# Performance work log

Hardware: AMD Instinct MI355X
Metric: run time of the kernel (lower is better)

Reference implementation:

```python
import jax, jax.numpy as jnp
import numpy as np

D_MODEL = 1024
NHEAD = 16
HEAD_DIM = D_MODEL // NHEAD
B, T = 2, 2048


def setup_inputs() -> dict:
    key = jax.random.key(0)
    ks = jax.random.split(key, 11)
    s = 1.0 / np.sqrt(D_MODEL)
    inp = {
        'q': jax.random.normal(ks[0], (B, T, D_MODEL), jnp.float32),
        'k': jax.random.normal(ks[1], (B, T, D_MODEL), jnp.float32),
        'v': jax.random.normal(ks[2], (B, T, D_MODEL), jnp.float32),
        'Wq': jax.random.normal(ks[3], (D_MODEL, D_MODEL), jnp.float32) * s,
        'bq': jnp.zeros((D_MODEL,), jnp.float32),
        'Wk': jax.random.normal(ks[4], (D_MODEL, D_MODEL), jnp.float32) * s,
        'bk': jnp.zeros((D_MODEL,), jnp.float32),
        'Wv': jax.random.normal(ks[5], (D_MODEL, D_MODEL), jnp.float32) * s,
        'bv': jnp.zeros((D_MODEL,), jnp.float32),
        'Wo': jax.random.normal(ks[6], (D_MODEL, D_MODEL), jnp.float32) * s,
        'bo': jnp.zeros((D_MODEL,), jnp.float32),
    }
    return inp


def reference(q, k, v, Wq, bq, Wk, bk, Wv, bv, Wo, bo):
    scale = np.sqrt(HEAD_DIM).astype(np.float32)
    # projections (torch Linear: x @ W.T + b), split heads -> [B, H, T, Dh]
    def proj(x, W, b):
        y = jnp.einsum('btd,ed->bte', x, W) + b
        return y.reshape(B, T, NHEAD, HEAD_DIM).transpose(0, 2, 1, 3)
    qh = proj(q, Wq, bq)
    kh = proj(k, Wk, bk)
    vh = proj(v, Wv, bv)
    scores = jnp.einsum('bhqd,bhkd->bhqk', qh, kh) / scale  # [B,H,T,T]
    weights = jax.nn.softmax(scores, axis=-1)
    out = jnp.einsum('bhqk,bhkd->bhqd', weights, vh)        # [B,H,T,Dh]
    out = out.transpose(0, 2, 1, 3).reshape(B, T, D_MODEL)
    return jnp.einsum('btd,ed->bte', out, Wo) + bo
```

## Files before the change

### kernel.cpp

```cpp
#include <hip/hip_runtime.h>
#include <cstdint>
#include <cstddef>


#define D_MODEL 1024
#define NHEAD   16
#define HDIM    64
#define BATCH   2
#define SEQ     2048
#define BT      (BATCH * SEQ)

#define QSCALE 0.18033688011112043f

typedef __bf16 bf16;
typedef __bf16 bf16x8 __attribute__((ext_vector_type(8)));
typedef __bf16 bf16x4 __attribute__((ext_vector_type(4)));
typedef float  floatx4 __attribute__((ext_vector_type(4)));
typedef short  short4v __attribute__((ext_vector_type(4)));

#define MFMA16(a, b, c) __builtin_amdgcn_mfma_f32_16x16x32_bf16((a), (b), (c), 0, 0, 0)

__device__ __forceinline__ floatx4 MFMA16B(bf16x4 a, bf16x4 b, floatx4 c) {
  return __builtin_amdgcn_mfma_f32_16x16x16bf16_1k(
      __builtin_bit_cast(short4v, a), __builtin_bit_cast(short4v, b), c, 0, 0, 0);
}

__device__ __forceinline__ float fexp2(float x) {
  return __builtin_amdgcn_exp2f(x);
}

__device__ __forceinline__ void async_cp16(const bf16* g, bf16* l) {
  __builtin_amdgcn_global_load_lds(
      (__attribute__((address_space(1))) void*)(g),
      (__attribute__((address_space(3))) void*)(l), 16, 0, 0);
}

__global__ __launch_bounds__(256) void cvt7(
    const float* __restrict__ s0, const float* __restrict__ s1,
    const float* __restrict__ s2, const float* __restrict__ s3,
    const float* __restrict__ s4, const float* __restrict__ s5,
    const float* __restrict__ s6,
    bf16* __restrict__ d0, bf16* __restrict__ d1, bf16* __restrict__ d2,
    bf16* __restrict__ d3, bf16* __restrict__ d4, bf16* __restrict__ d5,
    bf16* __restrict__ d6)
{
  const float* src; bf16* dst; int n4;
  switch (blockIdx.y) {
    case 0:  src = s0; dst = d0; n4 = (BT * D_MODEL) / 4; break;
    case 1:  src = s1; dst = d1; n4 = (BT * D_MODEL) / 4; break;
    case 2:  src = s2; dst = d2; n4 = (BT * D_MODEL) / 4; break;
    case 3:  src = s3; dst = d3; n4 = (D_MODEL * D_MODEL) / 4; break;
    case 4:  src = s4; dst = d4; n4 = (D_MODEL * D_MODEL) / 4; break;
    case 5:  src = s5; dst = d5; n4 = (D_MODEL * D_MODEL) / 4; break;
    default: src = s6; dst = d6; n4 = (D_MODEL * D_MODEL) / 4; break;
  }
  int stride = gridDim.x * blockDim.x;
  for (int i = blockIdx.x * blockDim.x + threadIdx.x; i < n4; i += stride) {
    float4 f = ((const float4*)src)[i];
    bf16x4 h;
    h[0] = (bf16)f.x; h[1] = (bf16)f.y; h[2] = (bf16)f.z; h[3] = (bf16)f.w;
    ((bf16x4*)dst)[i] = h;
  }
}

__device__ __forceinline__ void gemm128_core(
    const bf16* __restrict__ A, const bf16* __restrict__ W,
    int m0, int n0, bf16* As, bf16* Bs, floatx4 acc[4][4])
{
  const int t = threadIdx.x;
  const int l = t & 63, w = t >> 6;
  const int quad = l >> 4, lr = l & 15;
  const int wm = (w >> 1) * 64, wn = (w & 1) * 64;

  floatx4 z = {0.f, 0.f, 0.f, 0.f};
#pragma unroll
  for (int i = 0; i < 4; i++)
#pragma unroll
    for (int j = 0; j < 4; j++) acc[i][j] = z;

  for (int kt = 0; kt < 1024; kt += 32) {
    __syncthreads();
#pragma unroll
    for (int i = 0; i < 2; i++) {
      int c = i * 256 + t;
      int row = c >> 2, ci = c & 3;
      async_cp16(A + (size_t)(m0 + row) * 1024 + kt + ci * 8,
                 As + (i * 256 + w * 64) * 8);
      async_cp16(W + (size_t)(n0 + row) * 1024 + kt + ci * 8,
                 Bs + (i * 256 + w * 64) * 8);
    }
    __syncthreads();

    bf16x8 af[4], bfr[4];
#pragma unroll
    for (int i = 0; i < 4; i++) {
      af[i]  = *(const bf16x8*)(As + (wm + i * 16 + lr) * 32 + quad * 8);
      bfr[i] = *(const bf16x8*)(Bs + (wn + i * 16 + lr) * 32 + quad * 8);
    }
#pragma unroll
    for (int i = 0; i < 4; i++)
#pragma unroll
      for (int j = 0; j < 4; j++)
        acc[i][j] = MFMA16(af[i], bfr[j], acc[i][j]);
  }
}

__global__ __launch_bounds__(256) void qkv_gemm(
    const bf16* __restrict__ qb, const bf16* __restrict__ kb, const bf16* __restrict__ vb,
    const bf16* __restrict__ wq, const bf16* __restrict__ wk, const bf16* __restrict__ wv,
    const float* __restrict__ biasq, const float* __restrict__ biask, const float* __restrict__ biasv,
    bf16* __restrict__ qh, bf16* __restrict__ kh, bf16* __restrict__ vt)
{
  __shared__ bf16 As[128 * 32];
  __shared__ bf16 Bs[128 * 32];
  const int zid = blockIdx.z;
  const bf16* A = (zid == 0) ? qb : ((zid == 1) ? kb : vb);
  const bf16* W = (zid == 0) ? wq : ((zid == 1) ? wk : wv);
  const float* bias = (zid == 0) ? biasq : ((zid == 1) ? biask : biasv);
  const int m0 = blockIdx.x * 128, n0 = blockIdx.y * 128;

  floatx4 acc[4][4];
  gemm128_core(A, W, m0, n0, As, Bs, acc);

  const int t = threadIdx.x, l = t & 63, w = t >> 6;
  const int quad = l >> 4, lr = l & 15;
  const int wm = (w >> 1) * 64, wn = (w & 1) * 64;
  const float sc = (zid == 0) ? QSCALE : 1.0f;

  if (zid < 2) {
    bf16* out = (zid == 0) ? qh : kh;
#pragma unroll
    for (int i = 0; i < 4; i++) {
      int mbase = m0 + wm + i * 16 + quad * 4;
      int b  = mbase >> 11;
      int tq = mbase & 2047;
#pragma unroll
      for (int j = 0; j < 4; j++) {
        int n = n0 + wn + j * 16 + lr;
        float bv = bias[n];
        int h = n >> 6, dh = n & 63;
        bf16* p = out + ((size_t)((b * NHEAD + h) * SEQ + tq)) * HDIM + dh;
#pragma unroll
        for (int r = 0; r < 4; r++)
          p[(size_t)r * HDIM] = (bf16)((acc[i][j][r] + bv) * sc);
      }
    }
  } else {
#pragma unroll
    for (int i = 0; i < 4; i++) {
      int mbase = m0 + wm + i * 16 + quad * 4;
      int b  = mbase >> 11;
      int tq = mbase & 2047;
#pragma unroll
      for (int j = 0; j < 4; j++) {
        int n = n0 + wn + j * 16 + lr;
        float bv = bias[n];
        int h = n >> 6, dh = n & 63;
        bf16x4 pk;
#pragma unroll
        for (int r = 0; r < 4; r++) pk[r] = (bf16)(acc[i][j][r] + bv);
        *(bf16x4*)(vt + ((size_t)((b * NHEAD + h) * HDIM + dh)) * SEQ + tq) = pk;
      }
    }
  }
}

__global__ __launch_bounds__(256, 2) void attn_fused(
    const bf16* __restrict__ qh, const bf16* __restrict__ kh,
    const bf16* __restrict__ vt, bf16* __restrict__ attn)
{
  __shared__ __align__(16) char smem[65536];

  const int t = threadIdx.x, l = t & 63, w = t >> 6;
  const int quad = l >> 4, lr = l & 15;
  const int bh = blockIdx.y;
  const int qt0 = blockIdx.x * 128;
  const bf16* qg = qh + (size_t)bh * SEQ * HDIM;
  const bf16* kg = kh + (size_t)bh * SEQ * HDIM;
  const bf16* vg = vt + (size_t)bh * HDIM * SEQ;

  const bf16* kseg[4];
  const bf16* vseg[4];
#pragma unroll
  for (int i = 0; i < 4; i++) {
    int s = w * 4 + i;
    int krow = s * 8 + (l >> 3);
    kseg[i] = kg + (size_t)krow * HDIM + (((l & 7) ^ (l >> 3)) * 8);
    int vrow = s * 4 + (l >> 4);
    vseg[i] = vg + (size_t)vrow * SEQ + (((l & 15) ^ (vrow & 15)) * 8);
  }

  bf16x8 qf[2][2];
#pragma unroll
  for (int g = 0; g < 2; g++)
#pragma unroll
    for (int ko = 0; ko < 2; ko++)
      qf[g][ko] = *(const bf16x8*)(qg + (size_t)(qt0 + w * 32 + g * 16 + lr) * HDIM
                                   + ko * 32 + quad * 8);

  const floatx4 zz = {0.f, 0.f, 0.f, 0.f};
  floatx4 Oacc[2][4];
#pragma unroll
  for (int g = 0; g < 2; g++)
#pragma unroll
    for (int dt = 0; dt < 4; dt++) Oacc[g][dt] = zz;
  float mrow[2] = {-3.0e38f, -3.0e38f};
  float lrow[2] = {0.f, 0.f};

  auto stage = [&](int buf, int kt) {
    bf16* Kb = (bf16*)(smem + buf * 32768);
    bf16* Vb = (bf16*)(smem + buf * 32768 + 16384);
    int off = kt * 128;
#pragma unroll
    for (int i = 0; i < 4; i++) {
      async_cp16(kseg[i] + (size_t)off * HDIM, Kb + (w * 4 + i) * 512);
      async_cp16(vseg[i] + off,                Vb + (w * 4 + i) * 512);
    }
  };

  stage(0, 0);

  for (int kt = 0; kt < 16; kt++) {
    const int p = kt & 1;
    __syncthreads();
    if (kt + 1 < 16) stage(1 - p, kt + 1);
    const bf16* Ks  = (const bf16*)(smem + p * 32768);
    const bf16* Vts = (const bf16*)(smem + p * 32768 + 16384);

    const bf16* krow0 = Ks + lr * 64 + ((quad ^ (lr & 7)) * 8);
    const bf16* krow1 = Ks + lr * 64 + (((quad + 4) ^ (lr & 7)) * 8);

    floatx4 s0[8], s1[8];
#pragma unroll
    for (int ni = 0; ni < 8; ni++) {
      bf16x8 k0 = *(const bf16x8*)(krow0 + ni * 1024);
      bf16x8 k1 = *(const bf16x8*)(krow1 + ni * 1024);
      floatx4 a0 = MFMA16(k0, qf[0][0], zz);
      a0 = MFMA16(k1, qf[0][1], a0);
      floatx4 a1 = MFMA16(k0, qf[1][0], zz);
      a1 = MFMA16(k1, qf[1][1], a1);
      s0[ni] = a0;
      s1[ni] = a1;
    }

    bf16x4 pk0[8], pk1[8];
#pragma unroll
    for (int g = 0; g < 2; g++) {
      floatx4* sg = g ? s1 : s0;
      bf16x4* pkg = g ? pk1 : pk0;
      float rmax = sg[0][0];
#pragma unroll
      for (int ni = 0; ni < 8; ni++)
#pragma unroll
        for (int r = 0; r < 4; r++) rmax = fmaxf(rmax, sg[ni][r]);
      rmax = fmaxf(rmax, __shfl_xor(rmax, 16, 64));
      rmax = fmaxf(rmax, __shfl_xor(rmax, 32, 64));
      if (!__all(rmax - mrow[g] <= 8.0f)) {
        float mnew = fmaxf(mrow[g], rmax);
        float al = fexp2(mrow[g] - mnew);
        mrow[g] = mnew;
        lrow[g] *= al;
#pragma unroll
        for (int dt = 0; dt < 4; dt++)
#pragma unroll
          for (int r = 0; r < 4; r++) Oacc[g][dt][r] *= al;
      }
      float m = mrow[g];
      float rsum = 0.f;
#pragma unroll
      for (int ni = 0; ni < 8; ni++)
#pragma unroll
        for (int r = 0; r < 4; r++) {
          float pv = fexp2(sg[ni][r] - m);
          rsum += pv;
          pkg[ni][r] = (bf16)pv;
        }
      rsum += __shfl_xor(rsum, 16, 64);
      rsum += __shfl_xor(rsum, 32, 64);
      lrow[g] += rsum;
    }

    const bf16* vbase = Vts + lr * 128 + (quad & 1) * 4;
#pragma unroll
    for (int ni = 0; ni < 8; ni++) {
      const bf16* vp = vbase + (((ni * 2 + (quad >> 1)) ^ lr) * 8);
#pragma unroll
      for (int dt = 0; dt < 4; dt++) {
        bf16x4 vf = *(const bf16x4*)(vp + dt * 2048);
        Oacc[0][dt] = MFMA16B(vf, pk0[ni], Oacc[0][dt]);
        Oacc[1][dt] = MFMA16B(vf, pk1[ni], Oacc[1][dt]);
      }
    }
  }

  bf16* Ost = (bf16*)smem;
#pragma unroll
  for (int g = 0; g < 2; g++) {
    float inv = 1.0f / lrow[g];
#pragma unroll
    for (int dt = 0; dt < 4; dt++) {
      bf16x4 ov;
#pragma unroll
      for (int r = 0; r < 4; r++) ov[r] = (bf16)(Oacc[g][dt][r] * inv);
      *(bf16x4*)(Ost + (size_t)(w * 32 + g * 16 + lr) * 72 + dt * 16 + quad * 4) = ov;
    }
  }
  __syncthreads();

  const int b = bh >> 4, h = bh & 15;
#pragma unroll
  for (int i = 0; i < 4; i++) {
    int c = t + 256 * i;
    int row = c >> 3, ci = c & 7;
    *(int4*)(attn + ((size_t)b * SEQ + qt0 + row) * D_MODEL + h * HDIM + ci * 8) =
        *(const int4*)(Ost + row * 72 + ci * 8);
  }
}

__global__ __launch_bounds__(256) void oproj_gemm(
    const bf16* __restrict__ attn, const bf16* __restrict__ wo,
    const float* __restrict__ bo, float* __restrict__ out)
{
  __shared__ bf16 As[64 * 32];
  __shared__ bf16 Bs[64 * 32];
  const int m0 = blockIdx.x * 64, n0 = blockIdx.y * 64;
  const int t = threadIdx.x, l = t & 63, w = t >> 6;
  const int quad = l >> 4, lr = l & 15;
  const int wm = (w >> 1) * 32, wn = (w & 1) * 32;

  floatx4 z = {0.f, 0.f, 0.f, 0.f};
  floatx4 acc[2][2];
#pragma unroll
  for (int i = 0; i < 2; i++)
#pragma unroll
    for (int j = 0; j < 2; j++) acc[i][j] = z;

  for (int kt = 0; kt < 1024; kt += 32) {
    __syncthreads();
    {
      int row = t >> 2, ci = t & 3;
      async_cp16(attn + (size_t)(m0 + row) * 1024 + kt + ci * 8,
                 As + (w * 64) * 8);
      async_cp16(wo + (size_t)(n0 + row) * 1024 + kt + ci * 8,
                 Bs + (w * 64) * 8);
    }
    __syncthreads();

    bf16x8 af[2], bfr[2];
#pragma unroll
    for (int i = 0; i < 2; i++) {
      af[i]  = *(const bf16x8*)(As + (wm + i * 16 + lr) * 32 + quad * 8);
      bfr[i] = *(const bf16x8*)(Bs + (wn + i * 16 + lr) * 32 + quad * 8);
    }
#pragma unroll
    for (int i = 0; i < 2; i++)
#pragma unroll
      for (int j = 0; j < 2; j++)
        acc[i][j] = MFMA16(af[i], bfr[j], acc[i][j]);
  }

#pragma unroll
  for (int i = 0; i < 2; i++) {
    int m = m0 + wm + i * 16 + quad * 4;
#pragma unroll
    for (int j = 0; j < 2; j++) {
      int n = n0 + wn + j * 16 + lr;
      float bv = bo[n];
      float* p = out + (size_t)m * D_MODEL + n;
#pragma unroll
      for (int r = 0; r < 4; r++)
        p[(size_t)r * D_MODEL] = acc[i][j][r] + bv;
    }
  }
}

extern "C" void kernel_launch(void* const* d_in, const int* in_sizes, int n_in,
                              void* d_out, int out_size, void* d_ws, size_t ws_size,
                              hipStream_t stream)
{
  const float* q  = (const float*)d_in[0];
  const float* k  = (const float*)d_in[1];
  const float* v  = (const float*)d_in[2];
  const float* Wq = (const float*)d_in[3];
  const float* bq = (const float*)d_in[4];
  const float* Wk = (const float*)d_in[5];
  const float* bk = (const float*)d_in[6];
  const float* Wv = (const float*)d_in[7];
  const float* bv = (const float*)d_in[8];
  const float* Wo = (const float*)d_in[9];
  const float* bo = (const float*)d_in[10];

  const size_t NQ = (size_t)BT * D_MODEL;
  const size_t NW = (size_t)D_MODEL * D_MODEL;

  bf16* p = (bf16*)d_ws;
  bf16* qb   = p; p += NQ;
  bf16* kb   = p; p += NQ;
  bf16* vb   = p; p += NQ;
  bf16* wqb  = p; p += NW;
  bf16* wkb  = p; p += NW;
  bf16* wvb  = p; p += NW;
  bf16* wob  = p; p += NW;
  bf16* qhp  = p; p += NQ;
  bf16* khp  = p; p += NQ;
  bf16* vtp  = p; p += NQ;
  bf16* attn = p; p += NQ;

  cvt7<<<dim3(1024, 7, 1), 256, 0, stream>>>(q, k, v, Wq, Wk, Wv, Wo,
                                             qb, kb, vb, wqb, wkb, wvb, wob);
  qkv_gemm<<<dim3(32, 8, 3), 256, 0, stream>>>(qb, kb, vb, wqb, wkb, wvb,
                                               bq, bk, bv, qhp, khp, vtp);
  attn_fused<<<dim3(16, 32, 1), 256, 0, stream>>>(qhp, khp, vtp, attn);
  oproj_gemm<<<dim3(64, 16, 1), 256, 0, stream>>>(attn, wob, bo, (float*)d_out);
}
```

Measured before the change: 223.6 us.

## Remap attention blocks, interleave softmax reductions, and raise MFMA wave priority

Remaps the linear block index so that consecutive blocks cover different heads and batches at the same query tile. This is meant to change how K/V tiles are shared in L2 across concurrently running blocks. The softmax max and sum reductions are rewritten as tree reductions that handle both row groups together, giving the scheduler more independent work. MFMA sequences are wrapped in s_setprio and V fragment loads are hoisted so matrix ops issue back-to-back, while the reordered dependent MFMAs give more latency hiding. The risks are that the remapping assumes the grid is exactly 16 by 32 blocks, and that the priority hints may have little effect.

```diff
diff --git a/kernel.cpp b/kernel.cpp
--- a/kernel.cpp
+++ b/kernel.cpp
@@ -173,8 +173,12 @@
 
   const int t = threadIdx.x, l = t & 63, w = t >> 6;
   const int quad = l >> 4, lr = l & 15;
-  const int bh = blockIdx.y;
-  const int qt0 = blockIdx.x * 128;
+
+  const int hb  = blockIdx.y * 16 + blockIdx.x;
+  const int j   = hb >> 3;
+  const int bh  = (hb & 7) + ((j & 3) << 3);
+  const int qt0 = (j >> 2) * 128;
+
   const bf16* qg = qh + (size_t)bh * SEQ * HDIM;
   const bf16* kg = kh + (size_t)bh * SEQ * HDIM;
   const bf16* vg = vt + (size_t)bh * HDIM * SEQ;
@@ -235,61 +239,97 @@
     for (int ni = 0; ni < 8; ni++) {
       bf16x8 k0 = *(const bf16x8*)(krow0 + ni * 1024);
       bf16x8 k1 = *(const bf16x8*)(krow1 + ni * 1024);
+      __builtin_amdgcn_s_setprio(1);
       floatx4 a0 = MFMA16(k0, qf[0][0], zz);
+      floatx4 a1 = MFMA16(k0, qf[1][0], zz);
       a0 = MFMA16(k1, qf[0][1], a0);
-      floatx4 a1 = MFMA16(k0, qf[1][0], zz);
       a1 = MFMA16(k1, qf[1][1], a1);
+      __builtin_amdgcn_s_setprio(0);
       s0[ni] = a0;
       s1[ni] = a1;
     }
 
+    float xm0[8], xm1[8];
+#pragma unroll
+    for (int ni = 0; ni < 8; ni++) {
+      xm0[ni] = fmaxf(fmaxf(s0[ni][0], s0[ni][1]), fmaxf(s0[ni][2], s0[ni][3]));
+      xm1[ni] = fmaxf(fmaxf(s1[ni][0], s1[ni][1]), fmaxf(s1[ni][2], s1[ni][3]));
+    }
+    float r0 = fmaxf(fmaxf(fmaxf(xm0[0], xm0[1]), fmaxf(xm0[2], xm0[3])),
+                     fmaxf(fmaxf(xm0[4], xm0[5]), fmaxf(xm0[6], xm0[7])));
+    float r1 = fmaxf(fmaxf(fmaxf(xm1[0], xm1[1]), fmaxf(xm1[2], xm1[3])),
+                     fmaxf(fmaxf(xm1[4], xm1[5]), fmaxf(xm1[6], xm1[7])));
+    r0 = fmaxf(r0, __shfl_xor(r0, 16, 64));
+    r1 = fmaxf(r1, __shfl_xor(r1, 16, 64));
+    r0 = fmaxf(r0, __shfl_xor(r0, 32, 64));
+    r1 = fmaxf(r1, __shfl_xor(r1, 32, 64));
+
+    if (!__all(r0 - mrow[0] <= 8.0f)) {
+      float mnew = fmaxf(mrow[0], r0);
+      float al = fexp2(mrow[0] - mnew);
+      mrow[0] = mnew;
+      lrow[0] *= al;
+#pragma unroll
+      for (int dt = 0; dt < 4; dt++)
+#pragma unroll
+        for (int r = 0; r < 4; r++) Oacc[0][dt][r] *= al;
+    }
+    if (!__all(r1 - mrow[1] <= 8.0f)) {
+      float mnew = fmaxf(mrow[1], r1);
+      float al = fexp2(mrow[1] - mnew);
+      mrow[1] = mnew;
+      lrow[1] *= al;
+#pragma unroll
+      for (int dt = 0; dt < 4; dt++)
+#pragma unroll
+        for (int r = 0; r < 4; r++) Oacc[1][dt][r] *= al;
+    }
+
+    const float m0v = mrow[0], m1v = mrow[1];
     bf16x4 pk0[8], pk1[8];
-#pragma unroll
-    for (int g = 0; g < 2; g++) {
-      floatx4* sg = g ? s1 : s0;
-      bf16x4* pkg = g ? pk1 : pk0;
-      float rmax = sg[0][0];
-#pragma unroll
-      for (int ni = 0; ni < 8; ni++)
-#pragma unroll
-        for (int r = 0; r < 4; r++) rmax = fmaxf(rmax, sg[ni][r]);
-      rmax = fmaxf(rmax, __shfl_xor(rmax, 16, 64));
-      rmax = fmaxf(rmax, __shfl_xor(rmax, 32, 64));
-      if (!__all(rmax - mrow[g] <= 8.0f)) {
-        float mnew = fmaxf(mrow[g], rmax);
-        float al = fexp2(mrow[g] - mnew);
-        mrow[g] = mnew;
-        lrow[g] *= al;
-#pragma unroll
-        for (int dt = 0; dt < 4; dt++)
-#pragma unroll
-          for (int r = 0; r < 4; r++) Oacc[g][dt][r] *= al;
-      }
-      float m = mrow[g];
-      float rsum = 0.f;
-#pragma unroll
-      for (int ni = 0; ni < 8; ni++)
-#pragma unroll
-        for (int r = 0; r < 4; r++) {
-          float pv = fexp2(sg[ni][r] - m);
-          rsum += pv;
-          pkg[ni][r] = (bf16)pv;
-        }
-      rsum += __shfl_xor(rsum, 16, 64);
-      rsum += __shfl_xor(rsum, 32, 64);
-      lrow[g] += rsum;
-    }
+    float t0[8], t1[8];
+#pragma unroll
+    for (int ni = 0; ni < 8; ni++) {
+      float p00 = fexp2(s0[ni][0] - m0v), p01 = fexp2(s0[ni][1] - m0v);
+      float p02 = fexp2(s0[ni][2] - m0v), p03 = fexp2(s0[ni][3] - m0v);
+      float p10 = fexp2(s1[ni][0] - m1v), p11 = fexp2(s1[ni][1] - m1v);
+      float p12 = fexp2(s1[ni][2] - m1v), p13 = fexp2(s1[ni][3] - m1v);
+      pk0[ni][0] = (bf16)p00; pk0[ni][1] = (bf16)p01;
+      pk0[ni][2] = (bf16)p02; pk0[ni][3] = (bf16)p03;
+      pk1[ni][0] = (bf16)p10; pk1[ni][1] = (bf16)p11;
+      pk1[ni][2] = (bf16)p12; pk1[ni][3] = (bf16)p13;
+      t0[ni] = (p00 + p01) + (p02 + p03);
+      t1[ni] = (p10 + p11) + (p12 + p13);
+    }
+    float rs0 = ((t0[0] + t0[1]) + (t0[2] + t0[3]))
+              + ((t0[4] + t0[5]) + (t0[6] + t0[7]));
+    float rs1 = ((t1[0] + t1[1]) + (t1[2] + t1[3]))
+              + ((t1[4] + t1[5]) + (t1[6] + t1[7]));
+    rs0 += __shfl_xor(rs0, 16, 64);
+    rs1 += __shfl_xor(rs1, 16, 64);
+    rs0 += __shfl_xor(rs0, 32, 64);
+    rs1 += __shfl_xor(rs1, 32, 64);
+    lrow[0] += rs0;
+    lrow[1] += rs1;
 
     const bf16* vbase = Vts + lr * 128 + (quad & 1) * 4;
 #pragma unroll
     for (int ni = 0; ni < 8; ni++) {
       const bf16* vp = vbase + (((ni * 2 + (quad >> 1)) ^ lr) * 8);
-#pragma unroll
-      for (int dt = 0; dt < 4; dt++) {
-        bf16x4 vf = *(const bf16x4*)(vp + dt * 2048);
-        Oacc[0][dt] = MFMA16B(vf, pk0[ni], Oacc[0][dt]);
-        Oacc[1][dt] = MFMA16B(vf, pk1[ni], Oacc[1][dt]);
-      }
+      bf16x4 vf0 = *(const bf16x4*)(vp);
+      bf16x4 vf1 = *(const bf16x4*)(vp + 2048);
+      bf16x4 vf2 = *(const bf16x4*)(vp + 4096);
+      bf16x4 vf3 = *(const bf16x4*)(vp + 6144);
+      __builtin_amdgcn_s_setprio(1);
+      Oacc[0][0] = MFMA16B(vf0, pk0[ni], Oacc[0][0]);
+      Oacc[1][0] = MFMA16B(vf0, pk1[ni], Oacc[1][0]);
+      Oacc[0][1] = MFMA16B(vf1, pk0[ni], Oacc[0][1]);
+      Oacc[1][1] = MFMA16B(vf1, pk1[ni], Oacc[1][1]);
+      Oacc[0][2] = MFMA16B(vf2, pk0[ni], Oacc[0][2]);
+      Oacc[1][2] = MFMA16B(vf2, pk1[ni], Oacc[1][2]);
+      Oacc[0][3] = MFMA16B(vf3, pk0[ni], Oacc[0][3]);
+      Oacc[1][3] = MFMA16B(vf3, pk1[ni], Oacc[1][3]);
+      __builtin_amdgcn_s_setprio(0);
     }
   }
 
```

Result: no change. 227.1 us (+1.6%).
